# Performance work log

Measured on AMD Instinct MI355X. Metric: run time of the kernel, lower is better.

## Reference

```python
import jax, jax.numpy as jnp
import numpy as np

NUM_HEADS = 16
HEAD_DIM = 64
D_MODEL = NUM_HEADS * HEAD_DIM  # 1024
FEATURE_DIM = 2 * HEAD_DIM      # 128


def setup_inputs() -> dict:
    key = jax.random.key(0)
    ks = jax.random.split(key, 6)
    B, S = 4, 8192
    scale = D_MODEL ** -0.5
    x = jax.random.normal(ks[0], (B, S, D_MODEL), dtype=jnp.float32)
    Wq = jax.random.normal(ks[1], (D_MODEL, D_MODEL), dtype=jnp.float32) * scale
    Wk = jax.random.normal(ks[2], (D_MODEL, D_MODEL), dtype=jnp.float32) * scale
    Wv = jax.random.normal(ks[3], (D_MODEL, D_MODEL), dtype=jnp.float32) * scale
    Wo = jax.random.normal(ks[4], (D_MODEL, D_MODEL), dtype=jnp.float32) * scale
    # random_features buffer: [head_dim, feature_dim], scaled by head_dim**-0.5
    rf = jax.random.normal(ks[5], (HEAD_DIM, FEATURE_DIM), dtype=jnp.float32) * (HEAD_DIM ** -0.5)
    return {"x": x, "Wq": Wq, "Wk": Wk, "Wv": Wv, "Wo": Wo, "rf": rf}


def _phi(x, rf):
    # x: [B, H, S, head_dim] -> [B, H, S, feature_dim]
    proj = jnp.matmul(x, rf)  # [B, H, S, 2*head_dim]
    cos_p, sin_p = jnp.split(proj, 2, axis=-1)
    return jnp.concatenate([jnp.cos(cos_p), jnp.sin(sin_p)], axis=-1) * (FEATURE_DIM ** -0.5)


def reference(x, Wq, Wk, Wv, Wo, rf):
    B, S, _ = x.shape
    def heads(y):  # [B, S, D] -> [B, H, S, head_dim]
        return y.reshape(B, S, NUM_HEADS, HEAD_DIM).transpose(0, 2, 1, 3)
    Q = heads(x @ Wq)
    K = heads(x @ Wk)
    V = heads(x @ Wv)
    Qp = _phi(Q, rf)  # [B, H, S, F]
    Kp = _phi(K, rf)
    KV = jnp.einsum('bhsf,bhsd->bhfd', Kp, V)        # [B, H, F, head_dim]
    QKV = jnp.einsum('bhsf,bhfd->bhsd', Qp, KV)      # [B, H, S, head_dim]
    Z = jnp.einsum('bhsf,bhf->bhs', Qp, Kp.sum(axis=2))[..., None]
    Z = jnp.clip(Z, 1e-6, None)
    out = (QKV / Z).transpose(0, 2, 1, 3).reshape(B, S, D_MODEL)
    return out @ Wo
```

## Files before the change

kernel.cpp:

```cpp
#include <hip/hip_runtime.h>
#include <stdint.h>


#define DEVINL __device__ __forceinline__

typedef float f32x4 __attribute__((ext_vector_type(4)));
typedef __bf16 bf16x8 __attribute__((ext_vector_type(8)));
typedef unsigned short u16;

DEVINL u16 f2bf(float f) {
  union { float f; uint32_t u; } v; v.f = f;
  uint32_t u = v.u;
  u += 0x7fffu + ((u >> 16) & 1u);
  return (u16)(u >> 16);
}
DEVINL float bf2f(u16 h) {
  union { uint32_t u; float f; } v; v.u = ((uint32_t)h) << 16;
  return v.f;
}

#define GLOAD16(gp, lp) __builtin_amdgcn_global_load_lds( \
    (const __attribute__((address_space(1))) unsigned int*)(gp), \
    (__attribute__((address_space(3))) unsigned int*)(lp), 16, 0, 0)


DEVINL void stage_tile(const u16* gA, const u16* gB, u16* sl, int kt,
                       int wave, int lane) {
  const uint8_t* a8 = (const uint8_t*)gA + (size_t)kt * 64;
  const uint8_t* b8 = (const uint8_t*)gB + (size_t)kt * 64;
#pragma unroll
  for (int j = 0; j < 2; ++j) {
    int row = j * 128 + wave * 16 + (lane >> 2);
    int gch = (lane & 3) ^ ((row >> 2) & 3);
    GLOAD16(a8 + (size_t)row * 2048 + (size_t)gch * 16,
            (uint8_t*)sl + (size_t)(j * 128 + wave * 16) * 64);
    GLOAD16(b8 + (size_t)row * 2048 + (size_t)gch * 16,
            (uint8_t*)(sl + 8192) + (size_t)(j * 128 + wave * 16) * 64);
  }
}

DEVINL bf16x8 fragrd(const u16* base, int row, int lane) {
  int ch = (lane >> 4) ^ ((row >> 2) & 3);
  return *(const bf16x8*)&base[(size_t)row * 32 + ch * 8];
}

DEVINL void gemm_main(const u16* gA, const u16* gB, u16* smem,
                      f32x4 acc[8][4], int wave, int lane, int wr, int wc) {
  stage_tile(gA, gB, smem + 0 * 16384, 0, wave, lane);
  stage_tile(gA, gB, smem + 1 * 16384, 1, wave, lane);
  stage_tile(gA, gB, smem + 2 * 16384, 2, wave, lane);
  for (int t = 0; t < 32; ++t) {
    u16* sl = smem + (size_t)(t & 3) * 16384;
    if (t < 29) {
      stage_tile(gA, gB, smem + (size_t)((t + 3) & 3) * 16384, t + 3, wave, lane);
      asm volatile("s_waitcnt vmcnt(12)" ::: "memory");
    } else if (t == 29) {
      asm volatile("s_waitcnt vmcnt(8)" ::: "memory");
    } else if (t == 30) {
      asm volatile("s_waitcnt vmcnt(4)" ::: "memory");
    } else {
      asm volatile("s_waitcnt vmcnt(0)" ::: "memory");
    }
    __builtin_amdgcn_s_barrier();
    bf16x8 bfr[4];
#pragma unroll
    for (int n = 0; n < 4; ++n)
      bfr[n] = fragrd(sl + 8192, wc * 64 + n * 16 + (lane & 15), lane);
    __builtin_amdgcn_s_setprio(1);
#pragma unroll
    for (int am = 0; am < 8; ++am) {
      bf16x8 af = fragrd(sl, wr * 128 + am * 16 + (lane & 15), lane);
#pragma unroll
      for (int n = 0; n < 4; ++n)
        acc[am][n] = __builtin_amdgcn_mfma_f32_16x16x32_bf16(af, bfr[n], acc[am][n], 0, 0, 0);
    }
    __builtin_amdgcn_s_setprio(0);
    __builtin_amdgcn_s_barrier();
  }
}

template <int ROWS>
DEVINL void stage_r128(const uint8_t* g, size_t stride, u16* lds, int wave, int lane) {
#pragma unroll
  for (int j = 0; j < ROWS / 32; ++j) {
    int row = wave * (ROWS / 4) + j * 8 + (lane >> 3);
    GLOAD16(g + (size_t)row * stride + (size_t)(lane & 7) * 16,
            (uint8_t*)lds + (size_t)(wave * (ROWS / 4) + j * 8) * 128);
  }
}
template <int ROWS>
DEVINL void stage_r256(const uint8_t* g, size_t stride, u16* lds, int wave, int lane) {
#pragma unroll
  for (int j = 0; j < ROWS / 16; ++j) {
    int row = wave * (ROWS / 4) + j * 4 + (lane >> 4);
    GLOAD16(g + (size_t)row * stride + (size_t)(lane & 15) * 16,
            (uint8_t*)lds + (size_t)(wave * (ROWS / 4) + j * 4) * 256);
  }
}


__global__ __launch_bounds__(256) void cast_x_kernel(
    const float* __restrict__ src, u16* __restrict__ dst, long n4) {
  long i = (long)blockIdx.x * 256 + threadIdx.x;
  const long stride = (long)gridDim.x * 256;
  const float4* s4 = (const float4*)src;
  uint2* d4 = (uint2*)dst;
  for (; i < n4; i += stride) {
    float4 v = s4[i];
    uint2 o;
    o.x = (uint32_t)f2bf(v.x) | ((uint32_t)f2bf(v.y) << 16);
    o.y = (uint32_t)f2bf(v.z) | ((uint32_t)f2bf(v.w) << 16);
    d4[i] = o;
  }
}

__global__ __launch_bounds__(256) void transpose_cast_kernel(
    const float* __restrict__ src, u16* __restrict__ dst, int R, int C) {
  __shared__ float tile[32 * 33];
  const int ntr = R >> 5;
  const int tr = blockIdx.x % ntr, tc = blockIdx.x / ntr;
  const int tid = threadIdx.x;
  {
    int r = tid >> 3, c4 = (tid & 7) * 4;
    float4 v = *(const float4*)&src[(size_t)(tr * 32 + r) * C + tc * 32 + c4];
    tile[r * 33 + c4 + 0] = v.x;
    tile[r * 33 + c4 + 1] = v.y;
    tile[r * 33 + c4 + 2] = v.z;
    tile[r * 33 + c4 + 3] = v.w;
  }
  __syncthreads();
  {
    int c = tid >> 3, r4 = (tid & 7) * 4;
    uint2 o;
    o.x = (uint32_t)f2bf(tile[(r4 + 0) * 33 + c]) |
          ((uint32_t)f2bf(tile[(r4 + 1) * 33 + c]) << 16);
    o.y = (uint32_t)f2bf(tile[(r4 + 2) * 33 + c]) |
          ((uint32_t)f2bf(tile[(r4 + 3) * 33 + c]) << 16);
    *(uint2*)&dst[(size_t)(tc * 32 + c) * R + tr * 32 + r4] = o;
  }
}

__global__ __launch_bounds__(512, 2) void gemm_qkv_phi_kernel(
    const u16* __restrict__ xb, const u16* __restrict__ wT,
    const u16* __restrict__ rfT,
    u16* __restrict__ Qp, u16* __restrict__ KpT, u16* __restrict__ VhT) {
  __shared__ u16 smem[65536];
  const int tid = threadIdx.x, lane = tid & 63, wave = tid >> 6;
  const int wr = wave >> 2, wc = wave & 3;
  const int xcd = blockIdx.x & 7, ii = blockIdx.x >> 3;
  const int tn = ii % 12, tm = xcd * 16 + ii / 12;
  const int tensor = tn >> 2;

  f32x4 acc[8][4];
#pragma unroll
  for (int m = 0; m < 8; ++m)
#pragma unroll
    for (int n = 0; n < 4; ++n) acc[m][n] = (f32x4){0.f, 0.f, 0.f, 0.f};

  const u16* gA = xb + (size_t)tm * 256 * 1024;
  const u16* gB = wT + (size_t)tn * 256 * 1024;
  gemm_main(gA, gB, smem, acc, wave, lane, wr, wc);

  u16* patch = smem + (size_t)wave * 4608;
  const int b = tm >> 5;
  const int h = (tn & 3) * 4 + wc;
  const size_t bh = (size_t)b * 16 + h;
  const int sb = (tm & 31) * 256 + wr * 128;
  const float SC = 0.088388347648318447f;

  if (tensor == 2) {
#pragma unroll
    for (int sh = 0; sh < 2; ++sh) {
#pragma unroll
      for (int q = 0; q < 4; ++q)
#pragma unroll
        for (int n = 0; n < 4; ++n) {
          int d = n * 16 + (lane & 15);
          int s_l = q * 16 + (lane >> 4) * 4;
#pragma unroll
          for (int r = 0; r < 4; ++r)
            patch[d * 72 + s_l + r] = f2bf(acc[sh * 4 + q][n][r]);
        }
#pragma unroll
      for (int it = 0; it < 8; ++it) {
        int d = it * 8 + (lane >> 3);
        *(uint4*)&VhT[(bh * 64 + d) * 8192 + sb + sh * 64 + (lane & 7) * 8] =
            *(const uint4*)&patch[d * 72 + (lane & 7) * 8];
      }
    }
    return;
  }

#pragma unroll
  for (int ch = 0; ch < 2; ++ch) {
#pragma unroll
    for (int q = 0; q < 4; ++q)
#pragma unroll
      for (int n = 0; n < 4; ++n) {
        int d = n * 16 + (lane & 15);
        int s_l = q * 16 + (lane >> 4) * 4;
#pragma unroll
        for (int r = 0; r < 4; ++r)
          patch[(s_l + r) * 72 + d] = f2bf(acc[ch * 4 + q][n][r]);
      }
    bf16x8 af[4][2];
#pragma unroll
    for (int fm = 0; fm < 4; ++fm)
#pragma unroll
      for (int kk = 0; kk < 2; ++kk)
        af[fm][kk] = *(const bf16x8*)&patch[(size_t)(fm * 16 + (lane & 15)) * 72 +
                                            kk * 32 + (lane >> 4) * 8];
#pragma unroll
    for (int fh = 0; fh < 2; ++fh) {
      f32x4 pacc[4][4];
#pragma unroll
      for (int fm = 0; fm < 4; ++fm)
#pragma unroll
        for (int nn = 0; nn < 4; ++nn) pacc[fm][nn] = (f32x4){0.f, 0.f, 0.f, 0.f};
#pragma unroll
      for (int kk = 0; kk < 2; ++kk)
#pragma unroll
        for (int nn = 0; nn < 4; ++nn) {
          int f = (fh * 4 + nn) * 16 + (lane & 15);
          bf16x8 bb = *(const bf16x8*)&rfT[(size_t)f * 64 + kk * 32 + (lane >> 4) * 8];
#pragma unroll
          for (int fm = 0; fm < 4; ++fm)
            pacc[fm][nn] = __builtin_amdgcn_mfma_f32_16x16x32_bf16(af[fm][kk], bb, pacc[fm][nn], 0, 0, 0);
        }
#pragma unroll
      for (int fm = 0; fm < 4; ++fm)
#pragma unroll
        for (int nn = 0; nn < 4; ++nn) {
          int f_l = nn * 16 + (lane & 15);
          int s_l = fm * 16 + (lane >> 4) * 4;
#pragma unroll
          for (int r = 0; r < 4; ++r) {
            float pv = pacc[fm][nn][r];
            float v = (fh == 0 ? __cosf(pv) : __sinf(pv)) * SC;
            if (tensor == 0) patch[(s_l + r) * 72 + f_l] = f2bf(v);
            else             patch[f_l * 72 + s_l + r]   = f2bf(v);
          }
        }
      if (tensor == 0) {
#pragma unroll
        for (int it = 0; it < 8; ++it) {
          int s_l = it * 8 + (lane >> 3);
          *(uint4*)&Qp[(bh * 8192 + sb + ch * 64 + s_l) * 128 + fh * 64 + (lane & 7) * 8] =
              *(const uint4*)&patch[s_l * 72 + (lane & 7) * 8];
        }
      } else {
#pragma unroll
        for (int it = 0; it < 8; ++it) {
          int f_l = it * 8 + (lane >> 3);
          *(uint4*)&KpT[(bh * 128 + fh * 64 + f_l) * 8192 + sb + ch * 64 + (lane & 7) * 8] =
              *(const uint4*)&patch[f_l * 72 + (lane & 7) * 8];
        }
      }
    }
  }
}

__global__ __launch_bounds__(256) void kv_partial_kernel(
    const u16* __restrict__ KpT, const u16* __restrict__ VhT,
    float* __restrict__ partial) {
  __shared__ u16 smem2[12288];
  __shared__ float ksmem[256];
  u16* As = smem2;
  u16* Bs = smem2 + 8192;
  const int tid = threadIdx.x, lane = tid & 63, wave = tid >> 6;
  const int bh = blockIdx.x >> 3, ch = blockIdx.x & 7;
  const uint8_t* aB = (const uint8_t*)(KpT + (size_t)bh * 128 * 8192 + ch * 1024);
  const uint8_t* bB = (const uint8_t*)(VhT + (size_t)bh * 64 * 8192 + ch * 1024);

  f32x4 acc[2][4];
#pragma unroll
  for (int m = 0; m < 2; ++m)
#pragma unroll
    for (int n = 0; n < 4; ++n) acc[m][n] = (f32x4){0.f, 0.f, 0.f, 0.f};
  float ks = 0.f;
  const int fK = tid >> 1, sO = (tid & 1) * 32;

  for (int t = 0; t < 16; ++t) {
    stage_r128<128>(aB + t * 128, 16384, As, wave, lane);
    stage_r128<64>(bB + t * 128, 16384, Bs, wave, lane);
    __syncthreads();
#pragma unroll
    for (int i = 0; i < 4; ++i) {
      uint4 v = *(const uint4*)&As[fK * 64 + sO + i * 8];
      ks += bf2f((u16)(v.x & 0xffff)) + bf2f((u16)(v.x >> 16));
      ks += bf2f((u16)(v.y & 0xffff)) + bf2f((u16)(v.y >> 16));
      ks += bf2f((u16)(v.z & 0xffff)) + bf2f((u16)(v.z >> 16));
      ks += bf2f((u16)(v.w & 0xffff)) + bf2f((u16)(v.w >> 16));
    }
#pragma unroll
    for (int kk = 0; kk < 2; ++kk) {
      const int ko = kk * 32 + (lane >> 4) * 8;
      bf16x8 a[2], bb[4];
#pragma unroll
      for (int m = 0; m < 2; ++m)
        a[m] = *(const bf16x8*)&As[(size_t)(wave * 32 + m * 16 + (lane & 15)) * 64 + ko];
#pragma unroll
      for (int n = 0; n < 4; ++n)
        bb[n] = *(const bf16x8*)&Bs[(size_t)(n * 16 + (lane & 15)) * 64 + ko];
#pragma unroll
      for (int m = 0; m < 2; ++m)
#pragma unroll
        for (int n = 0; n < 4; ++n)
          acc[m][n] = __builtin_amdgcn_mfma_f32_16x16x32_bf16(a[m], bb[n], acc[m][n], 0, 0, 0);
    }
    __syncthreads();
  }

  float* pb = partial + (size_t)blockIdx.x * (128 * 65);
#pragma unroll
  for (int m = 0; m < 2; ++m)
#pragma unroll
    for (int n = 0; n < 4; ++n) {
      int d = n * 16 + (lane & 15);
#pragma unroll
      for (int r = 0; r < 4; ++r) {
        int f = wave * 32 + m * 16 + (lane >> 4) * 4 + r;
        pb[f * 65 + d] = acc[m][n][r];
      }
    }
  ksmem[tid] = ks;
  __syncthreads();
  if (tid < 128) pb[tid * 65 + 64] = ksmem[2 * tid] + ksmem[2 * tid + 1];
}

__global__ __launch_bounds__(256) void kv_reduce_kernel(
    const float* __restrict__ partial, u16* __restrict__ KVT) {
  const int bh = blockIdx.x, tid = threadIdx.x;
  for (int e = tid; e < 8320; e += 256) {
    float s = 0.f;
#pragma unroll
    for (int c = 0; c < 8; ++c) s += partial[(size_t)(bh * 8 + c) * 8320 + e];
    int f = e / 65, col = e % 65;
    KVT[((size_t)bh * 80 + col) * 128 + f] = f2bf(s);
  }
  for (int i = tid; i < 15 * 128; i += 256)
    KVT[((size_t)bh * 80 + 65) * 128 + i] = 0;
}

__global__ __launch_bounds__(256) void qkv_div_kernel(
    const u16* __restrict__ Qp, const u16* __restrict__ KVT, u16* __restrict__ A) {
  __shared__ u16 smem2[26624];
  u16* Qs = smem2;
  u16* Ks = smem2 + 16384;
  const int tid = threadIdx.x, lane = tid & 63, wave = tid >> 6;
  const int bh = blockIdx.x >> 6, st = blockIdx.x & 63;

  stage_r256<128>((const uint8_t*)(Qp + ((size_t)bh * 8192 + st * 128) * 128), 256,
                  Qs, wave, lane);
  stage_r256<80>((const uint8_t*)(KVT + (size_t)bh * 80 * 128), 256, Ks, wave, lane);
  __syncthreads();

  f32x4 acc[2][5];
#pragma unroll
  for (int m = 0; m < 2; ++m)
#pragma unroll
    for (int n = 0; n < 5; ++n) acc[m][n] = (f32x4){0.f, 0.f, 0.f, 0.f};

#pragma unroll
  for (int kk = 0; kk < 4; ++kk) {
    const int ko = kk * 32 + (lane >> 4) * 8;
    bf16x8 a[2], bb[5];
#pragma unroll
    for (int m = 0; m < 2; ++m)
      a[m] = *(const bf16x8*)&Qs[(size_t)(wave * 32 + m * 16 + (lane & 15)) * 128 + ko];
#pragma unroll
    for (int n = 0; n < 5; ++n)
      bb[n] = *(const bf16x8*)&Ks[(size_t)(n * 16 + (lane & 15)) * 128 + ko];
#pragma unroll
    for (int m = 0; m < 2; ++m)
#pragma unroll
      for (int n = 0; n < 5; ++n)
        acc[m][n] = __builtin_amdgcn_mfma_f32_16x16x32_bf16(a[m], bb[n], acc[m][n], 0, 0, 0);
  }

  const int b_ = bh >> 4, h = bh & 15;
#pragma unroll
  for (int m = 0; m < 2; ++m) {
#pragma unroll
    for (int r = 0; r < 4; ++r) {
      float z = fmaxf(__shfl(acc[m][4][r], lane & 48), 1e-6f);
      int srow = st * 128 + wave * 32 + m * 16 + (lane >> 4) * 4 + r;
      size_t rowb = ((size_t)b_ * 8192 + srow) * 1024 + h * 64;
#pragma unroll
      for (int n = 0; n < 4; ++n)
        A[rowb + n * 16 + (lane & 15)] = f2bf(acc[m][n][r] / z);
    }
  }
}

__global__ __launch_bounds__(512, 2) void gemm_out_kernel(
    const u16* __restrict__ A, const u16* __restrict__ WoT, float* __restrict__ out) {
  __shared__ u16 smem[65536];
  const int tid = threadIdx.x, lane = tid & 63, wave = tid >> 6;
  const int wr = wave >> 2, wc = wave & 3;
  const int xcd = blockIdx.x & 7, ii = blockIdx.x >> 3;
  const int tn = ii & 3, tm = xcd * 16 + (ii >> 2);

  f32x4 acc[8][4];
#pragma unroll
  for (int m = 0; m < 8; ++m)
#pragma unroll
    for (int n = 0; n < 4; ++n) acc[m][n] = (f32x4){0.f, 0.f, 0.f, 0.f};

  const u16* gA = A + (size_t)tm * 256 * 1024;
  const u16* gB = WoT + (size_t)tn * 256 * 1024;
  gemm_main(gA, gB, smem, acc, wave, lane, wr, wc);

  const int rowb = tm * 256 + wr * 128;
  const int colb = tn * 256 + wc * 64;
#pragma unroll
  for (int am = 0; am < 8; ++am)
#pragma unroll
    for (int n = 0; n < 4; ++n) {
      int row = rowb + am * 16 + (lane >> 4) * 4;
      int col = colb + n * 16 + (lane & 15);
#pragma unroll
      for (int r = 0; r < 4; ++r)
        out[(size_t)(row + r) * 1024 + col] = acc[am][n][r];
    }
}


extern "C" void kernel_launch(void* const* d_in, const int* in_sizes, int n_in,
                              void* d_out, int out_size, void* d_ws, size_t ws_size,
                              hipStream_t stream) {
  const float* x  = (const float*)d_in[0];
  const float* Wq = (const float*)d_in[1];
  const float* Wk = (const float*)d_in[2];
  const float* Wv = (const float*)d_in[3];
  const float* Wo = (const float*)d_in[4];
  const float* rf = (const float*)d_in[5];
  float* out = (float*)d_out;

  if (ws_size < (size_t)411058176) return;

  u16* ws = (u16*)d_ws;
  u16* xb    = ws;
  u16* Qp    = ws + 33554432UL;
  u16* KpT   = ws + 100663296UL;
  u16* VhT   = ws + 167772160UL;
  u16* wqkvT = ws + 201326592UL;
  u16* woT   = ws + 204472320UL;
  u16* rfT   = ws + 205520896UL;
  float* partial = (float*)xb;
  u16* KVT   = wqkvT;
  u16* Abuf  = xb;

  cast_x_kernel<<<4096, 256, 0, stream>>>(x, xb, 8388608L);
  transpose_cast_kernel<<<1024, 256, 0, stream>>>(Wq, wqkvT,            1024, 1024);
  transpose_cast_kernel<<<1024, 256, 0, stream>>>(Wk, wqkvT + 1048576,  1024, 1024);
  transpose_cast_kernel<<<1024, 256, 0, stream>>>(Wv, wqkvT + 2097152,  1024, 1024);
  transpose_cast_kernel<<<1024, 256, 0, stream>>>(Wo, woT,              1024, 1024);
  transpose_cast_kernel<<<8,    256, 0, stream>>>(rf, rfT,              64,   128);

  gemm_qkv_phi_kernel<<<1536, 512, 0, stream>>>(xb, wqkvT, rfT, Qp, KpT, VhT);
  kv_partial_kernel<<<512, 256, 0, stream>>>(KpT, VhT, partial);
  kv_reduce_kernel<<<64, 256, 0, stream>>>(partial, KVT);
  qkv_div_kernel<<<4096, 256, 0, stream>>>(Qp, KVT, Abuf);
  gemm_out_kernel<<<512, 512, 0, stream>>>(Abuf, woT, out);
}
```

Baseline: 620.9 us.

## Rework QKV GEMM pipeline, shrink output GEMM tiles, split KV partials finer

The QKV+phi GEMM drops the 4-stage 32-wide K pipeline in favour of a double-buffered 64-wide K tile. Each tile is staged in two halves, and the loads are interleaved across four MFMA phases with a rotated-slot LDS swizzle. The output GEMM moves from 256x256 tiles with 512 threads to 128x128 tiles with 256 threads and an XOR-swizzled single buffer. This gives more blocks, aiming for better occupancy and wave balance, but drops the software prefetch. The KV partial kernel splits the sequence into 16 chunks instead of 8 for more parallelism, at the cost of a larger reduction.

```diff
diff --git a/kernel.cpp b/kernel.cpp
--- a/kernel.cpp
+++ b/kernel.cpp
@@ -23,62 +23,6 @@
     (const __attribute__((address_space(1))) unsigned int*)(gp), \
     (__attribute__((address_space(3))) unsigned int*)(lp), 16, 0, 0)
 
-
-DEVINL void stage_tile(const u16* gA, const u16* gB, u16* sl, int kt,
-                       int wave, int lane) {
-  const uint8_t* a8 = (const uint8_t*)gA + (size_t)kt * 64;
-  const uint8_t* b8 = (const uint8_t*)gB + (size_t)kt * 64;
-#pragma unroll
-  for (int j = 0; j < 2; ++j) {
-    int row = j * 128 + wave * 16 + (lane >> 2);
-    int gch = (lane & 3) ^ ((row >> 2) & 3);
-    GLOAD16(a8 + (size_t)row * 2048 + (size_t)gch * 16,
-            (uint8_t*)sl + (size_t)(j * 128 + wave * 16) * 64);
-    GLOAD16(b8 + (size_t)row * 2048 + (size_t)gch * 16,
-            (uint8_t*)(sl + 8192) + (size_t)(j * 128 + wave * 16) * 64);
-  }
-}
-
-DEVINL bf16x8 fragrd(const u16* base, int row, int lane) {
-  int ch = (lane >> 4) ^ ((row >> 2) & 3);
-  return *(const bf16x8*)&base[(size_t)row * 32 + ch * 8];
-}
-
-DEVINL void gemm_main(const u16* gA, const u16* gB, u16* smem,
-                      f32x4 acc[8][4], int wave, int lane, int wr, int wc) {
-  stage_tile(gA, gB, smem + 0 * 16384, 0, wave, lane);
-  stage_tile(gA, gB, smem + 1 * 16384, 1, wave, lane);
-  stage_tile(gA, gB, smem + 2 * 16384, 2, wave, lane);
-  for (int t = 0; t < 32; ++t) {
-    u16* sl = smem + (size_t)(t & 3) * 16384;
-    if (t < 29) {
-      stage_tile(gA, gB, smem + (size_t)((t + 3) & 3) * 16384, t + 3, wave, lane);
-      asm volatile("s_waitcnt vmcnt(12)" ::: "memory");
-    } else if (t == 29) {
-      asm volatile("s_waitcnt vmcnt(8)" ::: "memory");
-    } else if (t == 30) {
-      asm volatile("s_waitcnt vmcnt(4)" ::: "memory");
-    } else {
-      asm volatile("s_waitcnt vmcnt(0)" ::: "memory");
-    }
-    __builtin_amdgcn_s_barrier();
-    bf16x8 bfr[4];
-#pragma unroll
-    for (int n = 0; n < 4; ++n)
-      bfr[n] = fragrd(sl + 8192, wc * 64 + n * 16 + (lane & 15), lane);
-    __builtin_amdgcn_s_setprio(1);
-#pragma unroll
-    for (int am = 0; am < 8; ++am) {
-      bf16x8 af = fragrd(sl, wr * 128 + am * 16 + (lane & 15), lane);
-#pragma unroll
-      for (int n = 0; n < 4; ++n)
-        acc[am][n] = __builtin_amdgcn_mfma_f32_16x16x32_bf16(af, bfr[n], acc[am][n], 0, 0, 0);
-    }
-    __builtin_amdgcn_s_setprio(0);
-    __builtin_amdgcn_s_barrier();
-  }
-}
-
 template <int ROWS>
 DEVINL void stage_r128(const uint8_t* g, size_t stride, u16* lds, int wave, int lane) {
 #pragma unroll
@@ -95,6 +39,47 @@
     int row = wave * (ROWS / 4) + j * 4 + (lane >> 4);
     GLOAD16(g + (size_t)row * stride + (size_t)(lane & 15) * 16,
             (uint8_t*)lds + (size_t)(wave * (ROWS / 4) + j * 4) * 256);
+  }
+}
+
+DEVINL void stage128_sw(const uint8_t* g, size_t stride, u16* lds, int wave, int lane) {
+  const int c = (lane & 7) ^ (lane >> 3);
+#pragma unroll
+  for (int j = 0; j < 4; ++j) {
+    int row = wave * 32 + j * 8 + (lane >> 3);
+    GLOAD16(g + (size_t)row * stride + (size_t)c * 16,
+            (uint8_t*)lds + (size_t)(wave * 32 + j * 8) * 128);
+  }
+}
+DEVINL void mma128_sw(const u16* As, const u16* Bs, f32x4 acc[4][4],
+                      int wr, int wc, int lane) {
+#pragma unroll
+  for (int kk = 0; kk < 2; ++kk) {
+    const int cw = kk * 4 + (lane >> 4);
+    const int sw = (cw ^ (lane & 7)) * 8;
+    bf16x8 a[4], b[4];
+#pragma unroll
+    for (int m = 0; m < 4; ++m)
+      a[m] = *(const bf16x8*)&As[(size_t)(wr * 64 + m * 16 + (lane & 15)) * 64 + sw];
+#pragma unroll
+    for (int n = 0; n < 4; ++n)
+      b[n] = *(const bf16x8*)&Bs[(size_t)(wc * 64 + n * 16 + (lane & 15)) * 64 + sw];
+#pragma unroll
+    for (int m = 0; m < 4; ++m)
+#pragma unroll
+      for (int n = 0; n < 4; ++n)
+        acc[m][n] = __builtin_amdgcn_mfma_f32_16x16x32_bf16(a[m], b[n], acc[m][n], 0, 0, 0);
+  }
+}
+
+DEVINL void stage_half(const u16* g, int koffB, u16* hb, int tid) {
+#pragma unroll
+  for (int l = 0; l < 2; ++l) {
+    int idx = l * 512 + tid;
+    int row = idx >> 2, sl = idx & 3;
+    int c = (sl - row - (row >> 2)) & 3;
+    GLOAD16((const uint8_t*)g + (size_t)row * 2048 + koffB + c * 16,
+            (uint8_t*)hb + (size_t)(idx & ~63) * 16);
   }
 }
 
@@ -150,16 +135,69 @@
   const int xcd = blockIdx.x & 7, ii = blockIdx.x >> 3;
   const int tn = ii % 12, tm = xcd * 16 + ii / 12;
   const int tensor = tn >> 2;
-
-  f32x4 acc[8][4];
-#pragma unroll
-  for (int m = 0; m < 8; ++m)
-#pragma unroll
-    for (int n = 0; n < 4; ++n) acc[m][n] = (f32x4){0.f, 0.f, 0.f, 0.f};
-
   const u16* gA = xb + (size_t)tm * 256 * 1024;
   const u16* gB = wT + (size_t)tn * 256 * 1024;
-  gemm_main(gA, gB, smem, acc, wave, lane, wr, wc);
+  const int slot4 = ((lane >> 4) + (lane & 3) + ((lane >> 2) & 3)) & 3;
+
+  f32x4 acc[8][4];
+#pragma unroll
+  for (int m = 0; m < 8; ++m)
+#pragma unroll
+    for (int n = 0; n < 4; ++n) acc[m][n] = (f32x4){0.f, 0.f, 0.f, 0.f};
+
+  stage_half(gA, 0, smem, tid);
+  stage_half(gB, 0, smem + 32768, tid);
+  stage_half(gA, 64, smem + 8192, tid);
+  stage_half(gB, 64, smem + 40960, tid);
+  asm volatile("s_waitcnt vmcnt(4)" ::: "memory");
+  __builtin_amdgcn_s_barrier();
+  asm volatile("" ::: "memory");
+
+  for (int t = 0; t < 16; ++t) {
+    const int buf = t & 1;
+    u16* Ab = smem + buf * 16384;
+    u16* Bb = smem + 32768 + buf * 16384;
+    u16* AbN = smem + (buf ^ 1) * 16384;
+    u16* BbN = smem + 32768 + (buf ^ 1) * 16384;
+    const int koffN = (t + 1) * 128;
+#pragma unroll
+    for (int p = 0; p < 4; ++p) {
+      const int ks = p >> 1, mh = p & 1;
+      const u16* Ah = Ab + ks * 8192;
+      const u16* Bh = Bb + ks * 8192;
+      bf16x8 bfr[4], afr[4];
+#pragma unroll
+      for (int n = 0; n < 4; ++n)
+        bfr[n] = *(const bf16x8*)&Bh[(size_t)(wc * 64 + n * 16 + (lane & 15)) * 32 + slot4 * 8];
+#pragma unroll
+      for (int m4 = 0; m4 < 4; ++m4)
+        afr[m4] = *(const bf16x8*)&Ah[(size_t)(wr * 128 + (mh * 4 + m4) * 16 + (lane & 15)) * 32 + slot4 * 8];
+      if (t < 15) {
+        if (p == 0) stage_half(gA, koffN,      AbN,        tid);
+        if (p == 1) stage_half(gB, koffN,      BbN,        tid);
+        if (p == 2) stage_half(gA, koffN + 64, AbN + 8192, tid);
+        if (p == 3) stage_half(gB, koffN + 64, BbN + 8192, tid);
+      }
+      if (p == 1) {
+        if (t == 15) asm volatile("s_waitcnt vmcnt(0)" ::: "memory");
+        else         asm volatile("s_waitcnt vmcnt(4)" ::: "memory");
+      } else if (p == 3) {
+        asm volatile("s_waitcnt vmcnt(4)" ::: "memory");
+      }
+      __builtin_amdgcn_s_barrier();
+      asm volatile("" ::: "memory");
+      __builtin_amdgcn_s_setprio(1);
+#pragma unroll
+      for (int m4 = 0; m4 < 4; ++m4)
+#pragma unroll
+        for (int n = 0; n < 4; ++n)
+          acc[mh * 4 + m4][n] =
+              __builtin_amdgcn_mfma_f32_16x16x32_bf16(afr[m4], bfr[n], acc[mh * 4 + m4][n], 0, 0, 0);
+      __builtin_amdgcn_s_setprio(0);
+      __builtin_amdgcn_s_barrier();
+      asm volatile("" ::: "memory");
+    }
+  }
 
   u16* patch = smem + (size_t)wave * 4608;
   const int b = tm >> 5;
@@ -268,9 +306,9 @@
   u16* As = smem2;
   u16* Bs = smem2 + 8192;
   const int tid = threadIdx.x, lane = tid & 63, wave = tid >> 6;
-  const int bh = blockIdx.x >> 3, ch = blockIdx.x & 7;
-  const uint8_t* aB = (const uint8_t*)(KpT + (size_t)bh * 128 * 8192 + ch * 1024);
-  const uint8_t* bB = (const uint8_t*)(VhT + (size_t)bh * 64 * 8192 + ch * 1024);
+  const int bh = blockIdx.x >> 4, ch = blockIdx.x & 15;
+  const uint8_t* aB = (const uint8_t*)(KpT + (size_t)bh * 128 * 8192 + ch * 512);
+  const uint8_t* bB = (const uint8_t*)(VhT + (size_t)bh * 64 * 8192 + ch * 512);
 
   f32x4 acc[2][4];
 #pragma unroll
@@ -280,7 +318,7 @@
   float ks = 0.f;
   const int fK = tid >> 1, sO = (tid & 1) * 32;
 
-  for (int t = 0; t < 16; ++t) {
+  for (int t = 0; t < 8; ++t) {
     stage_r128<128>(aB + t * 128, 16384, As, wave, lane);
     stage_r128<64>(bB + t * 128, 16384, Bs, wave, lane);
     __syncthreads();
@@ -334,7 +372,7 @@
   for (int e = tid; e < 8320; e += 256) {
     float s = 0.f;
 #pragma unroll
-    for (int c = 0; c < 8; ++c) s += partial[(size_t)(bh * 8 + c) * 8320 + e];
+    for (int c = 0; c < 16; ++c) s += partial[(size_t)(bh * 16 + c) * 8320 + e];
     int f = e / 65, col = e % 65;
     KVT[((size_t)bh * 80 + col) * 128 + f] = f2bf(s);
   }
@@ -393,35 +431,43 @@
   }
 }
 
-__global__ __launch_bounds__(512, 2) void gemm_out_kernel(
+__global__ __launch_bounds__(256, 3) void gemm_out_kernel(
     const u16* __restrict__ A, const u16* __restrict__ WoT, float* __restrict__ out) {
-  __shared__ u16 smem[65536];
+  __shared__ u16 smem[16384];
+  u16* As = smem;
+  u16* Bs = smem + 8192;
   const int tid = threadIdx.x, lane = tid & 63, wave = tid >> 6;
-  const int wr = wave >> 2, wc = wave & 3;
-  const int xcd = blockIdx.x & 7, ii = blockIdx.x >> 3;
-  const int tn = ii & 3, tm = xcd * 16 + (ii >> 2);
-
-  f32x4 acc[8][4];
-#pragma unroll
-  for (int m = 0; m < 8; ++m)
+  const int wr = wave >> 1, wc = wave & 1;
+  const int nb = (blockIdx.x & 7) * 256 + (blockIdx.x >> 3);
+  const int tn = nb & 7, tm = nb >> 3;
+
+  f32x4 acc[4][4];
+#pragma unroll
+  for (int m = 0; m < 4; ++m)
 #pragma unroll
     for (int n = 0; n < 4; ++n) acc[m][n] = (f32x4){0.f, 0.f, 0.f, 0.f};
 
-  const u16* gA = A + (size_t)tm * 256 * 1024;
-  const u16* gB = WoT + (size_t)tn * 256 * 1024;
-  gemm_main(gA, gB, smem, acc, wave, lane, wr, wc);
-
-  const int rowb = tm * 256 + wr * 128;
-  const int colb = tn * 256 + wc * 64;
-#pragma unroll
-  for (int am = 0; am < 8; ++am)
+  const uint8_t* aB = (const uint8_t*)(A + (size_t)tm * 128 * 1024);
+  const uint8_t* bB = (const uint8_t*)(WoT + (size_t)tn * 128 * 1024);
+  for (int kt = 0; kt < 16; ++kt) {
+    stage128_sw(aB + kt * 128, 2048, As, wave, lane);
+    stage128_sw(bB + kt * 128, 2048, Bs, wave, lane);
+    __syncthreads();
+    mma128_sw(As, Bs, acc, wr, wc, lane);
+    __syncthreads();
+  }
+
+  const int rowbase = tm * 128 + wr * 64;
+  const int colbase = tn * 128 + wc * 64;
+#pragma unroll
+  for (int m = 0; m < 4; ++m)
 #pragma unroll
     for (int n = 0; n < 4; ++n) {
-      int row = rowb + am * 16 + (lane >> 4) * 4;
-      int col = colb + n * 16 + (lane & 15);
+      int col = colbase + n * 16 + (lane & 15);
+      int row = rowbase + m * 16 + (lane >> 4) * 4;
 #pragma unroll
       for (int r = 0; r < 4; ++r)
-        out[(size_t)(row + r) * 1024 + col] = acc[am][n][r];
+        out[(size_t)(row + r) * 1024 + col] = acc[m][n][r];
     }
 }
 
@@ -459,8 +505,8 @@
   transpose_cast_kernel<<<8,    256, 0, stream>>>(rf, rfT,              64,   128);
 
   gemm_qkv_phi_kernel<<<1536, 512, 0, stream>>>(xb, wqkvT, rfT, Qp, KpT, VhT);
-  kv_partial_kernel<<<512, 256, 0, stream>>>(KpT, VhT, partial);
+  kv_partial_kernel<<<1024, 256, 0, stream>>>(KpT, VhT, partial);
   kv_reduce_kernel<<<64, 256, 0, stream>>>(partial, KVT);
   qkv_div_kernel<<<4096, 256, 0, stream>>>(Qp, KVT, Abuf);
-  gemm_out_kernel<<<512, 512, 0, stream>>>(Abuf, woT, out);
-}
+  gemm_out_kernel<<<2048, 256, 0, stream>>>(Abuf, woT, out);
+}
```

Result: slower. 633.4 us (+2.0%).
